# Performance work log

Measured on AMD Instinct MI355X. Metric: run time of the kernel, lower is better.

Reference implementation:

```python
import jax, jax.numpy as jnp
import numpy as np
from jax import lax

SEQ, B, NH, HD, NG = 1024, 16, 12, 64, 4  # gates: i, f, z, o (LSTM)


def setup_inputs() -> dict:
    key = jax.random.key(0)
    k1, k2 = jax.random.split(key)
    Wx = jax.random.normal(k1, (SEQ, B, NH, HD, NG), dtype=jnp.float32)
    states0 = jnp.zeros((2, B, NH, HD), dtype=jnp.float32)  # (h0, c0)
    # scale recurrent weights for stability (like 1/sqrt(head_dim) init)
    R = jax.random.normal(k2, (NH, NG, HD, HD), dtype=jnp.float32) / jnp.sqrt(jnp.float32(HD))
    b = jnp.zeros((NH, NG, HD), dtype=jnp.float32)
    return {"Wx": Wx, "states0": states0, "R": R, "b": b}


def reference(Wx, states0, R, b):
    # Wx: [T, B, N, D, G] -> [T, B, N, G, D]
    Wx_g = jnp.swapaxes(Wx, -1, -2)
    h0, c0 = states0[0], states0[1]

    def step(carry, x_t):
        h, c = carry
        # per-head recurrent gate pre-activations: [B, N, G, D]
        g = x_t + jnp.einsum('ngod,bnd->bngo', R, h) + b
        i = jax.nn.sigmoid(g[:, :, 0])
        f = jax.nn.sigmoid(g[:, :, 1])
        z = jnp.tanh(g[:, :, 2])
        o = jax.nn.sigmoid(g[:, :, 3])
        c = f * c + i * z
        h = o * jnp.tanh(c)
        return (h, c), (h, c)

    _, (hs, cs) = lax.scan(step, (h0, c0), Wx_g)
    # states: [num_states=2, T+1, B, N, D] (initial state included, as in flashrnn)
    h_all = jnp.concatenate([h0[None], hs], axis=0)
    c_all = jnp.concatenate([c0[None], cs], axis=0)
    return jnp.stack([h_all, c_all], axis=0)
```

## Files before the change

### kernel.cpp

```cpp
#include <hip/hip_runtime.h>


#define T_SEQ 1024
#define B_    16
#define NH_   12
#define HD_   64
#define NG_   4
#define BN_   (B_*NH_)
#define WX_T_STRIDE (BN_*HD_*NG_)
#define OUT_T_STRIDE (BN_*HD_)
#define OUT_S_STRIDE ((T_SEQ+1)*OUT_T_STRIDE)

typedef float v4f __attribute__((ext_vector_type(4)));

#define LDS_BARRIER() asm volatile("s_waitcnt lgkmcnt(0)\n\ts_barrier" ::: "memory")

#define PIN4(x) asm volatile("" : "+v"(x))
#define PIN1(x) asm volatile("" : "+v"(x))

#define QXOR(x, CTRL) \
    __int_as_float(__builtin_amdgcn_update_dpp(0, __float_as_int(x), (CTRL), 0xF, 0xF, true))

__global__ __launch_bounds__(256, 1) __attribute__((amdgpu_waves_per_eu(1)))
void flashrnn_lstm_fwd(const float* __restrict__ Wx,
                       const float* __restrict__ s0,
                       const float* __restrict__ R,
                       const float* __restrict__ bias,
                       float* __restrict__ out)
{
    const int bid = blockIdx.x;
    const int n   = bid % NH_;
    const int b   = bid / NH_;
    const int bn  = b*NH_ + n;
    const int tid = threadIdx.x;
    const int o   = tid >> 2;
    const int g   = tid & 3;

    __shared__ float hbuf[2][64];

    const v4f* Rp = (const v4f*)(R + ((size_t)((n*NG_ + g)*HD_ + o)) * HD_);
    v4f r0 = Rp[0],  r1 = Rp[1],  r2 = Rp[2],  r3 = Rp[3];
    v4f r4 = Rp[4],  r5 = Rp[5],  r6 = Rp[6],  r7 = Rp[7];
    v4f r8 = Rp[8],  r9 = Rp[9],  r10 = Rp[10], r11 = Rp[11];
    v4f r12 = Rp[12], r13 = Rp[13], r14 = Rp[14], r15 = Rp[15];
    PIN4(r0);  PIN4(r1);  PIN4(r2);  PIN4(r3);
    PIN4(r4);  PIN4(r5);  PIN4(r6);  PIN4(r7);
    PIN4(r8);  PIN4(r9);  PIN4(r10); PIN4(r11);
    PIN4(r12); PIN4(r13); PIN4(r14); PIN4(r15);

    float bval = bias[(n*NG_ + g)*HD_ + o];
    PIN1(bval);

    float c = s0[BN_*HD_ + bn*HD_ + o];

    if (tid < 128) {
        const int d = tid & 63;
        const size_t sofs = (tid < 64) ? (size_t)0 : (size_t)OUT_S_STRIDE;
        const float v = (tid < 64) ? s0[bn*HD_ + d] : s0[BN_*HD_ + bn*HD_ + d];
        if (tid < 64) hbuf[0][d] = v;
        out[sofs + (size_t)bn*HD_ + d] = v;
    }

    const bool isg1 = (g & 1) != 0;
    float* stp = out + (isg1 ? (size_t)OUT_S_STRIDE : (size_t)0)
                     + (size_t)OUT_T_STRIDE + (size_t)bn*HD_ + o;

    const float s_coef = (g == 2) ? -2.88539008f : -1.44269504f;
    const float m_coef = (g == 2) ? 2.0f : 1.0f;
    const float a_coef = (g == 2) ? -1.0f : 0.0f;

    const float* wxp = Wx + (size_t)bn*(HD_*NG_) + tid;
    float wx0 = wxp[0];
    float wx1 = wxp[(size_t)1 * WX_T_STRIDE];
    float wx2 = wxp[(size_t)2 * WX_T_STRIDE];
    float wx3 = wxp[(size_t)3 * WX_T_STRIDE];

    __syncthreads();

#define DOT(R4, H4)                                                            \
        acc.x = fmaf((R4).x, (H4).x, acc.x);                                   \
        acc.y = fmaf((R4).y, (H4).y, acc.y);                                   \
        acc.z = fmaf((R4).z, (H4).z, acc.z);                                   \
        acc.w = fmaf((R4).w, (H4).w, acc.w);

#define STEP(TT, SLOT, CUR)                                                    \
    {                                                                          \
        const float wxv = wx##SLOT;                                            \
        { int tl = tb + (TT) + 4; if (tl > T_SEQ-1) tl = T_SEQ-1;              \
          wx##SLOT = wxp[(size_t)tl * WX_T_STRIDE]; }                          \
        v4f acc = {0.f, 0.f, 0.f, 0.f};                                        \
        const v4f* hv = (const v4f*)&hbuf[CUR][0];                             \
        const v4f h0 = hv[0],  h1 = hv[1],  h2 = hv[2],  h3 = hv[3];           \
        const v4f h4 = hv[4],  h5 = hv[5],  h6 = hv[6],  h7 = hv[7];           \
        const v4f h8 = hv[8],  h9 = hv[9],  h10 = hv[10], h11 = hv[11];        \
        const v4f h12 = hv[12], h13 = hv[13], h14 = hv[14], h15 = hv[15];      \
        DOT(r0,h0)  DOT(r1,h1)  DOT(r2,h2)  DOT(r3,h3)                         \
        DOT(r4,h4)  DOT(r5,h5)  DOT(r6,h6)  DOT(r7,h7)                         \
        DOT(r8,h8)  DOT(r9,h9)  DOT(r10,h10) DOT(r11,h11)                      \
        DOT(r12,h12) DOT(r13,h13) DOT(r14,h14) DOT(r15,h15)                    \
        const float gp = ((acc.x+acc.y)+(acc.z+acc.w)) + wxv + bval;           \
        const float ev = __builtin_amdgcn_exp2f(s_coef * gp);                  \
        const float rv = __builtin_amdgcn_rcpf(1.0f + ev);                     \
        const float a  = fmaf(m_coef, rv, a_coef);                             \
        const float v1 = QXOR(a, 0xB1);                          \
        const float v2 = QXOR(a, 0x4E);                          \
        const float v3 = QXOR(a, 0x1B);                          \
         \
        const float xf = isg1 ? a  : v1;                                       \
        const float xi = isg1 ? v1 : a;                                        \
        const float xz = isg1 ? v3 : v2;                                       \
        const float xo = isg1 ? v2 : v3;                                       \
        c = fmaf(xf, c, xi * xz);                                              \
        const float e2 = __builtin_amdgcn_exp2f(-2.88539008f * c);             \
        const float th = fmaf(2.0f, __builtin_amdgcn_rcpf(1.0f + e2), -1.0f);  \
        const float hval = xo * th;                                            \
        if (g == 0) hbuf[(CUR)^1][o] = hval;                                   \
        if (g < 2) { *stp = isg1 ? c : hval; stp += OUT_T_STRIDE; }            \
        LDS_BARRIER();                                                         \
    }

    for (int tb = 0; tb < T_SEQ; tb += 4) {
        STEP(0, 0, 0)
        STEP(1, 1, 1)
        STEP(2, 2, 0)
        STEP(3, 3, 1)
    }
#undef STEP
#undef DOT
}

extern "C" void kernel_launch(void* const* d_in, const int* in_sizes, int n_in,
                              void* d_out, int out_size, void* d_ws, size_t ws_size,
                              hipStream_t stream) {
    const float* Wx = (const float*)d_in[0];
    const float* s0 = (const float*)d_in[1];
    const float* R  = (const float*)d_in[2];
    const float* bb = (const float*)d_in[3];
    float* out = (float*)d_out;
    flashrnn_lstm_fwd<<<dim3(BN_), dim3(256), 0, stream>>>(Wx, s0, R, bb, out);
}
```

Measured before the change: 673.6 us.

## Split recurrent dot product across the quad and reduce partial sums with DPP

Each lane in a 4-lane quad now reads only a 16-element slice of h from LDS instead of all 64, and computes partial dot products for all four gates of its output unit using R slices loaded at gate offsets g^k. The partials are combined across the quad with DPP swizzles, so each lane ends up holding the full pre-activation for its own gate. This cuts per-step LDS reads by 4x while keeping the same FMA count. In exchange it adds a serial 16-FMA chain per gate plus DPP reduction latency on the critical recurrence path. The hbuf array is also padded and aligned.

```diff
diff --git a/kernel.cpp b/kernel.cpp
--- a/kernel.cpp
+++ b/kernel.cpp
@@ -21,6 +21,20 @@
 #define QXOR(x, CTRL) \
     __int_as_float(__builtin_amdgcn_update_dpp(0, __float_as_int(x), (CTRL), 0xF, 0xF, true))
 
+__device__ __forceinline__ float dot16(v4f a0, v4f a1, v4f a2, v4f a3,
+                                       v4f h0, v4f h1, v4f h2, v4f h3)
+{
+    float p = a0.x * h0.x;
+    p = fmaf(a0.y, h0.y, p); p = fmaf(a0.z, h0.z, p); p = fmaf(a0.w, h0.w, p);
+    p = fmaf(a1.x, h1.x, p); p = fmaf(a1.y, h1.y, p);
+    p = fmaf(a1.z, h1.z, p); p = fmaf(a1.w, h1.w, p);
+    p = fmaf(a2.x, h2.x, p); p = fmaf(a2.y, h2.y, p);
+    p = fmaf(a2.z, h2.z, p); p = fmaf(a2.w, h2.w, p);
+    p = fmaf(a3.x, h3.x, p); p = fmaf(a3.y, h3.y, p);
+    p = fmaf(a3.z, h3.z, p); p = fmaf(a3.w, h3.w, p);
+    return p;
+}
+
 __global__ __launch_bounds__(256, 1) __attribute__((amdgpu_waves_per_eu(1)))
 void flashrnn_lstm_fwd(const float* __restrict__ Wx,
                        const float* __restrict__ s0,
@@ -36,17 +50,22 @@
     const int o   = tid >> 2;
     const int g   = tid & 3;
 
-    __shared__ float hbuf[2][64];
+    __shared__ __align__(16) float hbuf[2][80];
 
-    const v4f* Rp = (const v4f*)(R + ((size_t)((n*NG_ + g)*HD_ + o)) * HD_);
-    v4f r0 = Rp[0],  r1 = Rp[1],  r2 = Rp[2],  r3 = Rp[3];
-    v4f r4 = Rp[4],  r5 = Rp[5],  r6 = Rp[6],  r7 = Rp[7];
-    v4f r8 = Rp[8],  r9 = Rp[9],  r10 = Rp[10], r11 = Rp[11];
-    v4f r12 = Rp[12], r13 = Rp[13], r14 = Rp[14], r15 = Rp[15];
-    PIN4(r0);  PIN4(r1);  PIN4(r2);  PIN4(r3);
-    PIN4(r4);  PIN4(r5);  PIN4(r6);  PIN4(r7);
-    PIN4(r8);  PIN4(r9);  PIN4(r10); PIN4(r11);
-    PIN4(r12); PIN4(r13); PIN4(r14); PIN4(r15);
+    const size_t rowstride = (size_t)HD_*HD_;
+    const float* Rh = R + (size_t)n*NG_*rowstride + (size_t)o*HD_ + g*16;
+    const v4f* RpA = (const v4f*)(Rh + (size_t)(g^0)*rowstride);
+    const v4f* RpB = (const v4f*)(Rh + (size_t)(g^1)*rowstride);
+    const v4f* RpC = (const v4f*)(Rh + (size_t)(g^2)*rowstride);
+    const v4f* RpD = (const v4f*)(Rh + (size_t)(g^3)*rowstride);
+    v4f r00 = RpA[0], r01 = RpA[1], r02 = RpA[2], r03 = RpA[3];
+    v4f r10 = RpB[0], r11 = RpB[1], r12 = RpB[2], r13 = RpB[3];
+    v4f r20 = RpC[0], r21 = RpC[1], r22 = RpC[2], r23 = RpC[3];
+    v4f r30 = RpD[0], r31 = RpD[1], r32 = RpD[2], r33 = RpD[3];
+    PIN4(r00); PIN4(r01); PIN4(r02); PIN4(r03);
+    PIN4(r10); PIN4(r11); PIN4(r12); PIN4(r13);
+    PIN4(r20); PIN4(r21); PIN4(r22); PIN4(r23);
+    PIN4(r30); PIN4(r31); PIN4(r32); PIN4(r33);
 
     float bval = bias[(n*NG_ + g)*HD_ + o];
     PIN1(bval);
@@ -77,28 +96,30 @@
 
     __syncthreads();
 
-#define DOT(R4, H4)                                                            \
-        acc.x = fmaf((R4).x, (H4).x, acc.x);                                   \
-        acc.y = fmaf((R4).y, (H4).y, acc.y);                                   \
-        acc.z = fmaf((R4).z, (H4).z, acc.z);                                   \
-        acc.w = fmaf((R4).w, (H4).w, acc.w);
-
 #define STEP(TT, SLOT, CUR)                                                    \
     {                                                                          \
+                      \
+        asm volatile("" :: "v"(r00), "v"(r01), "v"(r02), "v"(r03),             \
+                           "v"(r10), "v"(r11), "v"(r12), "v"(r13),             \
+                           "v"(r20), "v"(r21), "v"(r22), "v"(r23),             \
+                           "v"(r30), "v"(r31), "v"(r32), "v"(r33));            \
         const float wxv = wx##SLOT;                                            \
         { int tl = tb + (TT) + 4; if (tl > T_SEQ-1) tl = T_SEQ-1;              \
           wx##SLOT = wxp[(size_t)tl * WX_T_STRIDE]; }                          \
-        v4f acc = {0.f, 0.f, 0.f, 0.f};                                        \
-        const v4f* hv = (const v4f*)&hbuf[CUR][0];                             \
-        const v4f h0 = hv[0],  h1 = hv[1],  h2 = hv[2],  h3 = hv[3];           \
-        const v4f h4 = hv[4],  h5 = hv[5],  h6 = hv[6],  h7 = hv[7];           \
-        const v4f h8 = hv[8],  h9 = hv[9],  h10 = hv[10], h11 = hv[11];        \
-        const v4f h12 = hv[12], h13 = hv[13], h14 = hv[14], h15 = hv[15];      \
-        DOT(r0,h0)  DOT(r1,h1)  DOT(r2,h2)  DOT(r3,h3)                         \
-        DOT(r4,h4)  DOT(r5,h5)  DOT(r6,h6)  DOT(r7,h7)                         \
-        DOT(r8,h8)  DOT(r9,h9)  DOT(r10,h10) DOT(r11,h11)                      \
-        DOT(r12,h12) DOT(r13,h13) DOT(r14,h14) DOT(r15,h15)                    \
-        const float gp = ((acc.x+acc.y)+(acc.z+acc.w)) + wxv + bval;           \
+           \
+        const v4f* hv = (const v4f*)&hbuf[CUR][g*16];                          \
+        const v4f ha = hv[0], hb = hv[1], hcq = hv[2], hd = hv[3];             \
+               \
+        float p0 = dot16(r00, r01, r02, r03, ha, hb, hcq, hd);                 \
+        float p1 = dot16(r10, r11, r12, r13, ha, hb, hcq, hd);                 \
+        float p2 = dot16(r20, r21, r22, r23, ha, hb, hcq, hd);                 \
+        float p3 = dot16(r30, r31, r32, r33, ha, hb, hcq, hd);                 \
+                                          \
+            \
+        const float q0 = p0 + QXOR(p1, 0xB1);                                  \
+        const float q2 = p2 + QXOR(p3, 0xB1);                                  \
+        const float d0 = q0 + QXOR(q2, 0x4E);          \
+        const float gp = d0 + wxv + bval;                                      \
         const float ev = __builtin_amdgcn_exp2f(s_coef * gp);                  \
         const float rv = __builtin_amdgcn_rcpf(1.0f + ev);                     \
         const float a  = fmaf(m_coef, rv, a_coef);                             \
@@ -126,7 +147,6 @@
         STEP(3, 3, 1)
     }
 #undef STEP
-#undef DOT
 }
 
 extern "C" void kernel_launch(void* const* d_in, const int* in_sizes, int n_in,
```

Measured after the change: 583.8 us. 1.15x faster.
